# Kernel optimization log

Measured on AMD Instinct MI355X. Metric: run time of the kernel, lower is better.

## Reference

```python
import jax, jax.numpy as jnp
import numpy as np

WEIGHT = 1.0  # init kwarg `weight`
BOX = 5      # half-size of the text box in pixels


def setup_inputs() -> dict:
    key = jax.random.key(0)
    k1, k2, k3, k4 = jax.random.split(key, 4)
    B, C, H, W, T = 32, 4, 512, 512, 64
    return {
        "predicted_noise": jax.random.normal(k1, (B, C, H, W), dtype=jnp.float32),
        "target_noise": jax.random.normal(k2, (B, C, H, W), dtype=jnp.float32),
        "text_tokens": jax.random.randint(k3, (B, T), 0, 50000, dtype=jnp.int64),
        "text_positions": jax.random.uniform(k4, (B, T, 2), dtype=jnp.float32),
    }


def _text_mask(text_positions, H, W, dtype):
    # text_positions: [B, T, 2] normalized (x, y). A valid token (x>0, y>0)
    # paints a [y_pos-5, y_pos+5) x [x_pos-5, x_pos+5) box of ones (clipped to image).
    x = text_positions[..., 0]
    y = text_positions[..., 1]
    valid = (x > 0) & (y > 0)                              # [B, T]
    x_pos = jnp.floor(x * W).astype(jnp.int32)             # int(x*W), x>0 so floor==trunc
    y_pos = jnp.floor(y * H).astype(jnp.int32)
    ii = jnp.arange(H, dtype=jnp.int32)                    # rows; clipping is implicit
    jj = jnp.arange(W, dtype=jnp.int32)
    cond_y = valid[..., None] & (ii >= y_pos[..., None] - BOX) & (ii < y_pos[..., None] + BOX)  # [B,T,H]
    cond_x = (jj >= x_pos[..., None] - BOX) & (jj < x_pos[..., None] + BOX)                      # [B,T,W]
    # union over tokens of the outer-product boxes, via a small matmul over T
    hits = jnp.einsum('bti,btj->bij', cond_y.astype(dtype), cond_x.astype(dtype))  # [B,H,W]
    return (hits > 0).astype(dtype)


def reference(predicted_noise, target_noise, text_tokens, text_positions):
    diff2 = (predicted_noise - target_noise) ** 2
    base_loss = jnp.mean(diff2)
    _, _, H, W = predicted_noise.shape
    mask = _text_mask(text_positions, H, W, predicted_noise.dtype)   # [B,H,W]
    text_weight = 1.0 + 3.0 * mask[:, None, :, :]                    # [B,1,H,W]
    text_loss = jnp.mean(text_weight * diff2)
    return base_loss + WEIGHT * (text_loss - base_loss)
```

## Files before the change

kernel.cpp:

```cpp
#include <hip/hip_runtime.h>

#define Bb 32
#define Cc 4
#define Hh 512
#define Ww 512
#define Tt 64
#define HW (Hh * Ww)
#define NTOT ((long long)Bb * Cc * Hh * Ww)
#define NQUAD (Bb * HW / 4)

#define GRID2 2048
#define ITER2 (NQUAD / (GRID2 * 256))

#define ROWMASK_OFF 65536

__global__ __launch_bounds__(256) void build_rowmask_kernel(
    const float* __restrict__ pos,
    unsigned long long* __restrict__ rowmask)
{
    int row = blockIdx.x * 256 + threadIdx.x;
    if (row >= Bb * Hh) return;
    int b = row >> 9;
    int h = row & 511;

    unsigned long long m[8];
#pragma unroll
    for (int i = 0; i < 8; ++i) m[i] = 0ull;

    const float* p = pos + (size_t)b * Tt * 2;
    for (int t = 0; t < Tt; ++t) {
        float x = p[2 * t + 0];
        float y = p[2 * t + 1];
        if (!(x > 0.0f && y > 0.0f)) continue;
        int xp = (int)floorf(x * (float)Ww);
        int yp = (int)floorf(y * (float)Hh);
        if (h < yp - 5 || h >= yp + 5) continue;
        int xlo = xp - 5; if (xlo < 0) xlo = 0;
        int xhi = xp + 5; if (xhi > Ww) xhi = Ww;
        if (xlo >= xhi) continue;
        int w0 = xlo >> 6;
        int w1 = (xhi - 1) >> 6;
        for (int wd = w0; wd <= w1; ++wd) {
            int lo = xlo - (wd << 6); if (lo < 0) lo = 0;
            int hi = xhi - (wd << 6); if (hi > 64) hi = 64;
            m[wd] |= (((1ull << (hi - lo)) - 1ull) << lo);
        }
    }

    unsigned long long* out = rowmask + (size_t)row * 8;
#pragma unroll
    for (int i = 0; i < 8; ++i) out[i] = m[i];
}

__global__ __launch_bounds__(256, 8) void weighted_sq_sum_kernel(
    const float* __restrict__ pred,
    const float* __restrict__ targ,
    const unsigned long long* __restrict__ rowmask,
    double* __restrict__ partials)
{
    const int tid0 = blockIdx.x * 256 + threadIdx.x;
    const int PS = HW / 4;

    double acc = 0.0;
#pragma unroll
    for (int it = 0; it < ITER2; ++it) {
        int gid = tid0 + it * (GRID2 * 256);
        int b   = gid >> 16;
        int rem = gid & 65535;
        int h   = rem >> 7;
        int w   = (rem & 127) << 2;

        size_t base = (size_t)b * (Cc * HW) + (size_t)h * Ww + (size_t)w;
        const float4* p4 = (const float4*)(pred + base);
        const float4* t4 = (const float4*)(targ + base);

        unsigned long long word = rowmask[((size_t)b * Hh + h) * 8 + (w >> 6)];
        unsigned bits = (unsigned)((word >> (w & 63)) & 0xFull);

        float sx = 0.f, sy = 0.f, sz = 0.f, sw = 0.f;
#pragma unroll
        for (int c = 0; c < Cc; ++c) {
            float4 a = p4[(size_t)c * PS];
            float4 t = t4[(size_t)c * PS];
            float dx = a.x - t.x, dy = a.y - t.y, dz = a.z - t.z, dw = a.w - t.w;
            sx += dx * dx; sy += dy * dy; sz += dz * dz; sw += dw * dw;
        }

        float tot  = sx + sy + sz + sw;
        float msum = (bits & 1u ? sx : 0.f) + (bits & 2u ? sy : 0.f) +
                     (bits & 4u ? sz : 0.f) + (bits & 8u ? sw : 0.f);
        acc += (double)tot + 3.0 * (double)msum;
    }

#pragma unroll
    for (int off = 32; off > 0; off >>= 1)
        acc += __shfl_down(acc, off, 64);

    __shared__ double lsum[4];
    int lane = threadIdx.x & 63;
    int wid  = threadIdx.x >> 6;
    if (lane == 0) lsum[wid] = acc;
    __syncthreads();
    if (threadIdx.x == 0)
        partials[blockIdx.x] = lsum[0] + lsum[1] + lsum[2] + lsum[3];
}

__global__ __launch_bounds__(256) void final_reduce_kernel(
    const double* __restrict__ partials, float* __restrict__ out)
{
    double v = 0.0;
    for (int i = threadIdx.x; i < GRID2; i += 256) v += partials[i];
#pragma unroll
    for (int off = 32; off > 0; off >>= 1)
        v += __shfl_down(v, off, 64);
    __shared__ double lsum[4];
    int lane = threadIdx.x & 63;
    int wid  = threadIdx.x >> 6;
    if (lane == 0) lsum[wid] = v;
    __syncthreads();
    if (threadIdx.x == 0)
        out[0] = (float)((lsum[0] + lsum[1] + lsum[2] + lsum[3]) * (1.0 / (double)NTOT));
}

extern "C" void kernel_launch(void* const* d_in, const int* in_sizes, int n_in,
                              void* d_out, int out_size, void* d_ws, size_t ws_size,
                              hipStream_t stream) {
    const float* pred = (const float*)d_in[0];
    const float* targ = (const float*)d_in[1];
    const float* pos  = (const float*)d_in[3];

    double* partials = (double*)d_ws;
    unsigned long long* rowmask =
        (unsigned long long*)((char*)d_ws + ROWMASK_OFF);
    float* out = (float*)d_out;

    build_rowmask_kernel<<<(Bb * Hh + 255) / 256, 256, 0, stream>>>(pos, rowmask);

    weighted_sq_sum_kernel<<<GRID2, 256, 0, stream>>>(pred, targ, rowmask, partials);

    final_reduce_kernel<<<1, 256, 0, stream>>>(partials, out);
}
```

Before: 289.3 us.

## Issue all streaming loads up front via inline asm with staged waitcnt consumption

Rewrites the weighted squared-sum kernel so each thread handles 8 contiguous float4 quads (one per batch-channel slab) at a fixed stride. All rowmask, pred and targ loads are issued first as raw global_load instructions with 32-bit offsets, then consumed in order behind decreasing vmcnt waits. The grid doubles and occupancy is lowered to 4 waves per SIMD so each thread can hold more loads in flight. It relies on hand-written asm and manual waitcnt counting. The mask is now reloaded per channel instead of once per pixel.

```diff
diff --git a/kernel.cpp b/kernel.cpp
--- a/kernel.cpp
+++ b/kernel.cpp
@@ -7,12 +7,15 @@
 #define Tt 64
 #define HW (Hh * Ww)
 #define NTOT ((long long)Bb * Cc * Hh * Ww)
-#define NQUAD (Bb * HW / 4)
+#define QTOT (Bb * Cc * HW / 4)
 
-#define GRID2 2048
-#define ITER2 (NQUAD / (GRID2 * 256))
+#define GRID2 4096
+#define THREADS2 (GRID2 * 256)
+#define KPT 8
 
 #define ROWMASK_OFF 65536
+
+typedef float f32x4 __attribute__((ext_vector_type(4)));
 
 __global__ __launch_bounds__(256) void build_rowmask_kernel(
     const float* __restrict__ pos,
@@ -52,45 +55,63 @@
     for (int i = 0; i < 8; ++i) out[i] = m[i];
 }
 
-__global__ __launch_bounds__(256, 8) void weighted_sq_sum_kernel(
+__global__ __launch_bounds__(256, 4) void weighted_sq_sum_kernel(
     const float* __restrict__ pred,
     const float* __restrict__ targ,
     const unsigned long long* __restrict__ rowmask,
     double* __restrict__ partials)
 {
-    const int tid0 = blockIdx.x * 256 + threadIdx.x;
-    const int PS = HW / 4;
+    const int tid = blockIdx.x * 256 + (int)threadIdx.x;
+
+    const unsigned vo0 = (unsigned)tid * 16u;
+    const unsigned ro0 =
+        (((unsigned)(tid >> 18) * 512u + (unsigned)((tid >> 7) & 511)) * 8u
+         + (unsigned)((tid >> 4) & 7)) * 8u;
+    const unsigned sh = (unsigned)((tid & 15) << 2);
+
+    unsigned long long rm[KPT];
+    f32x4 pv[KPT], tv[KPT];
+
+#pragma unroll
+    for (int k = 0; k < KPT; ++k) {
+        unsigned ro = ro0 + (unsigned)k * 131072u;
+        asm volatile("global_load_dwordx2 %0, %1, %2"
+                     : "=&v"(rm[k]) : "v"(ro), "s"(rowmask));
+    }
+#pragma unroll
+    for (int k = 0; k < KPT; ++k) {
+        unsigned vo = vo0 + (unsigned)k * 16777216u;
+        asm volatile("global_load_dwordx4 %0, %1, %2"
+                     : "=&v"(pv[k]) : "v"(vo), "s"(pred));
+        asm volatile("global_load_dwordx4 %0, %1, %2"
+                     : "=&v"(tv[k]) : "v"(vo), "s"(targ));
+    }
 
     double acc = 0.0;
-#pragma unroll
-    for (int it = 0; it < ITER2; ++it) {
-        int gid = tid0 + it * (GRID2 * 256);
-        int b   = gid >> 16;
-        int rem = gid & 65535;
-        int h   = rem >> 7;
-        int w   = (rem & 127) << 2;
 
-        size_t base = (size_t)b * (Cc * HW) + (size_t)h * Ww + (size_t)w;
-        const float4* p4 = (const float4*)(pred + base);
-        const float4* t4 = (const float4*)(targ + base);
+#define CONSUME(k, n)                                                         \
+    {                                                                         \
+        asm volatile("s_waitcnt vmcnt(" #n ")" ::: "memory");                 \
+        __builtin_amdgcn_sched_barrier(0);                                    \
+        f32x4 a = pv[k], t = tv[k];                                           \
+        float dx = a.x - t.x, dy = a.y - t.y, dz = a.z - t.z, dw = a.w - t.w; \
+        float sx = dx * dx, sy = dy * dy, sz = dz * dz, sw = dw * dw;         \
+        unsigned bits = (unsigned)((rm[k] >> sh) & 0xFull);                   \
+        float tot  = sx + sy + sz + sw;                                       \
+        float msum = (bits & 1u ? sx : 0.f) + (bits & 2u ? sy : 0.f) +        \
+                     (bits & 4u ? sz : 0.f) + (bits & 8u ? sw : 0.f);         \
+        acc += (double)tot + 3.0 * (double)msum;                              \
+    }
 
-        unsigned long long word = rowmask[((size_t)b * Hh + h) * 8 + (w >> 6)];
-        unsigned bits = (unsigned)((word >> (w & 63)) & 0xFull);
-
-        float sx = 0.f, sy = 0.f, sz = 0.f, sw = 0.f;
-#pragma unroll
-        for (int c = 0; c < Cc; ++c) {
-            float4 a = p4[(size_t)c * PS];
-            float4 t = t4[(size_t)c * PS];
-            float dx = a.x - t.x, dy = a.y - t.y, dz = a.z - t.z, dw = a.w - t.w;
-            sx += dx * dx; sy += dy * dy; sz += dz * dz; sw += dw * dw;
-        }
-
-        float tot  = sx + sy + sz + sw;
-        float msum = (bits & 1u ? sx : 0.f) + (bits & 2u ? sy : 0.f) +
-                     (bits & 4u ? sz : 0.f) + (bits & 8u ? sw : 0.f);
-        acc += (double)tot + 3.0 * (double)msum;
-    }
+    CONSUME(0, 14)
+    CONSUME(1, 12)
+    CONSUME(2, 10)
+    CONSUME(3, 8)
+    CONSUME(4, 6)
+    CONSUME(5, 4)
+    CONSUME(6, 2)
+    CONSUME(7, 0)
+#undef CONSUME
 
 #pragma unroll
     for (int off = 32; off > 0; off >>= 1)
```

Result: slower. 312.3 us (+7.9%).
